# Performance work log

Measured on AMD Instinct MI355X. Metric: run time of the kernel, lower is better.

The kernel has to match this reference:

```python
import jax, jax.numpy as jnp
import numpy as np

B, L, DM, H = 2, 2048, 512, 8
D = DM // H
FACTOR = 5
NUM_K = int(FACTOR * np.ceil(np.log(L)))  # 40
NUM_Q = NUM_K  # q_len == k_len here
EPS = 1e-5


def setup_inputs() -> dict:
    key = jax.random.key(0)
    ks = jax.random.split(key, 12)
    s = DM ** -0.5
    return {
        "q": jax.random.normal(ks[0], (B, L, DM), jnp.float32),
        "k": jax.random.normal(ks[1], (B, L, DM), jnp.float32),
        "v": jax.random.normal(ks[2], (B, L, DM), jnp.float32),
        "Wq": jax.random.normal(ks[3], (DM, DM), jnp.float32) * s,
        "bq": jnp.zeros((DM,), jnp.float32),
        "Wk": jax.random.normal(ks[4], (DM, DM), jnp.float32) * s,
        "bk": jnp.zeros((DM,), jnp.float32),
        "Wv": jax.random.normal(ks[5], (DM, DM), jnp.float32) * s,
        "bv": jnp.zeros((DM,), jnp.float32),
        "gamma": jnp.ones((DM,), jnp.float32),
        "beta": jnp.zeros((DM,), jnp.float32),
        "random_index": jax.random.randint(ks[6], (L, NUM_K), 0, L, jnp.int32),
    }


def _heads(x):
    # [B, L, DM] -> [B, H, L, D]
    return x.reshape(B, L, H, D).transpose(0, 2, 1, 3)


def reference(q, k, v, Wq, bq, Wk, bk, Wv, bv, gamma, beta, random_index):
    qp = _heads(q @ Wq + bq)
    kp = _heads(k @ Wk + bk)
    vp = _heads(v @ Wv + bv)

    # ProbSparse: sample NUM_K keys per query position (shared over batch/head)
    k_samp = kp[:, :, random_index, :]                      # [B,H,L,NUM_K,D]
    pre = jnp.einsum('bhid,bhijd->bhij', qp, k_samp)        # [B,H,L,NUM_K]
    measure = pre.max(-1) - pre.sum(-1) / L                 # sparsity measure [B,H,L]
    _, q_idx = jax.lax.top_k(measure, NUM_Q)                # [B,H,NUM_Q]

    q_sel = jnp.take_along_axis(qp, q_idx[..., None], axis=2)   # [B,H,NUM_Q,D]
    attn = jnp.einsum('bhid,bhjd->bhij', q_sel, kp) * D ** -0.5 # [B,H,NUM_Q,L]
    attn = jax.nn.softmax(attn, axis=-1)                    # dropout = identity (eval)
    out_sel = jnp.einsum('bhij,bhjd->bhid', attn, vp)       # [B,H,NUM_Q,D]

    # use_mask=False path: context is the mean of v over keys
    v_mean = vp.mean(axis=2)                                # [B,H,D]
    context = jnp.broadcast_to(v_mean[:, :, None, :], (B, H, L, D))
    bi = jnp.arange(B)[:, None, None]
    hi = jnp.arange(H)[None, :, None]
    out = context.at[bi, hi, q_idx].set(out_sel)            # scatter selected rows

    out = out.transpose(0, 2, 1, 3).reshape(B, L, DM)
    y = out + q
    mu = y.mean(-1, keepdims=True)
    var = y.var(-1, keepdims=True)
    yn = (y - mu) / jnp.sqrt(var + EPS) * gamma + beta
    return (yn, attn)
```

## Files before the change

### kernel.cpp

```cpp
#include <hip/hip_runtime.h>
#include <math.h>

#define BB 2
#define LL 2048
#define DMM 512
#define HH 8
#define DD 64
#define NUMK 40
#define NUMQ 40
#define LNEPS 1e-5f
#define LSEG 512
#define NLS 4

typedef unsigned short ushort_t;
typedef __attribute__((ext_vector_type(8))) short bf16x8;
typedef __attribute__((ext_vector_type(4))) float f32x4;

__device__ inline ushort_t f2bf(float x) {
    union { float f; unsigned int u; } v; v.f = x;
    unsigned int r = v.u + 0x7fffu + ((v.u >> 16) & 1u);
    return (ushort_t)(r >> 16);
}
__device__ inline float bf2f(ushort_t h) {
    union { unsigned int u; float f; } v; v.u = ((unsigned int)h) << 16;
    return v.f;
}

__global__ __launch_bounds__(256) void convert_x_kernel(
    const float* __restrict__ q, const float* __restrict__ k, const float* __restrict__ v,
    ushort_t* __restrict__ Xh, ushort_t* __restrict__ Xl) {
    const size_t plane = (size_t)BB * LL * DMM;
    const float* X = (blockIdx.y == 0) ? q : (blockIdx.y == 1) ? k : v;
    ushort_t* xh = Xh + plane * blockIdx.y;
    ushort_t* xl = Xl + plane * blockIdx.y;
    const size_t base = ((size_t)blockIdx.x * 256 + threadIdx.x) * 8;
    float4 a = *(const float4*)(X + base);
    float4 b = *(const float4*)(X + base + 4);
    float xs[8] = {a.x, a.y, a.z, a.w, b.x, b.y, b.z, b.w};
    unsigned int hp[4], lp[4];
#pragma unroll
    for (int j = 0; j < 4; ++j) {
        ushort_t h0 = f2bf(xs[2 * j]),     h1 = f2bf(xs[2 * j + 1]);
        ushort_t l0 = f2bf(xs[2 * j] - bf2f(h0));
        ushort_t l1 = f2bf(xs[2 * j + 1] - bf2f(h1));
        hp[j] = (unsigned int)h0 | ((unsigned int)h1 << 16);
        lp[j] = (unsigned int)l0 | ((unsigned int)l1 << 16);
    }
    *(uint4*)(xh + base) = make_uint4(hp[0], hp[1], hp[2], hp[3]);
    *(uint4*)(xl + base) = make_uint4(lp[0], lp[1], lp[2], lp[3]);
}

__global__ __launch_bounds__(256) void convert_w_kernel(
    const float* __restrict__ Wq, const float* __restrict__ Wk, const float* __restrict__ Wv,
    ushort_t* __restrict__ Wht, ushort_t* __restrict__ Wlt) {
    __shared__ float tile[64][65];
    const size_t plane = (size_t)DMM * DMM;
    const float* W = (blockIdx.z == 0) ? Wq : (blockIdx.z == 1) ? Wk : Wv;
    ushort_t* wht = Wht + plane * blockIdx.z;
    ushort_t* wlt = Wlt + plane * blockIdx.z;
    const int n0 = blockIdx.x * 64, k0 = blockIdx.y * 64;
    const int t = threadIdx.x;
    const int d = t & 63, g = t >> 6;
    for (int rr = g; rr < 64; rr += 4)
        tile[rr][d] = W[(size_t)(k0 + rr) * DMM + n0 + d];
    __syncthreads();
    for (int cc = g; cc < 64; cc += 4) {
        float x = tile[d][cc];
        ushort_t hi = f2bf(x);
        ushort_t lo = f2bf(x - bf2f(hi));
        wht[(size_t)(n0 + cc) * DMM + k0 + d] = hi;
        wlt[(size_t)(n0 + cc) * DMM + k0 + d] = lo;
    }
}

__device__ inline void stage_one(const ushort_t* __restrict__ g, ushort_t* lbuf,
                                 int r0, int lane, int k0) {
    const int r = r0 + (lane >> 3);
    const int c = (lane & 7) ^ (r & 7);
    const ushort_t* gp = g + (size_t)r * DMM + k0 + c * 8;
    __builtin_amdgcn_global_load_lds(
        (const __attribute__((address_space(1))) unsigned int*)gp,
        (__attribute__((address_space(3))) unsigned int*)(lbuf + (size_t)r0 * 64),
        16, 0, 0);
}
__device__ inline bf16x8 frag_ld(const ushort_t* buf, int row, int c) {
    const int idx = row * 8 + (c ^ (row & 7));
    return *(const bf16x8*)(buf + idx * 8);
}

__global__ __launch_bounds__(256) void proj_mfma_kernel(
    const ushort_t* __restrict__ Xh, const ushort_t* __restrict__ Xl,
    const ushort_t* __restrict__ Wht, const ushort_t* __restrict__ Wlt,
    const float* __restrict__ bq, const float* __restrict__ bk, const float* __restrict__ bv,
    float* __restrict__ Oq, float* __restrict__ Ok, float* __restrict__ Ov) {
    const int z = blockIdx.z;
    const size_t xplane = (size_t)BB * LL * DMM;
    const size_t wplane = (size_t)DMM * DMM;
    const ushort_t* ah_g = Xh + xplane * z;
    const ushort_t* al_g = Xl + xplane * z;
    const ushort_t* bh_g = Wht + wplane * z;
    const ushort_t* bl_g = Wlt + wplane * z;
    const float* bias = (z == 0) ? bq : (z == 1) ? bk : bv;
    float* Out = (z == 0) ? Oq : (z == 1) ? Ok : Ov;

    __shared__ __align__(16) ushort_t bufAh[64 * 64];
    __shared__ __align__(16) ushort_t bufAl[64 * 64];
    __shared__ __align__(16) ushort_t bufBh[64 * 64];
    __shared__ __align__(16) ushort_t bufBl[64 * 64];

    const int t = threadIdx.x;
    const int lane = t & 63, w = t >> 6;
    const int wm = (w & 1) * 32, wn = (w >> 1) * 32;
    const int m0 = blockIdx.x * 64, j0 = blockIdx.y * 64;

    const ushort_t* A_h = ah_g + (size_t)m0 * DMM;
    const ushort_t* A_l = al_g + (size_t)m0 * DMM;
    const ushort_t* B_h = bh_g + (size_t)j0 * DMM;
    const ushort_t* B_l = bl_g + (size_t)j0 * DMM;

    f32x4 acc[2][2];
#pragma unroll
    for (int i = 0; i < 2; ++i)
#pragma unroll
        for (int j = 0; j < 2; ++j) acc[i][j] = (f32x4){0.f, 0.f, 0.f, 0.f};

    for (int ch = 0; ch < 8; ++ch) {
        const int k0 = ch * 64;
#pragma unroll
        for (int i = 0; i < 2; ++i) {
            const int r0 = (w * 2 + i) * 8;
            stage_one(A_h, bufAh, r0, lane, k0);
            stage_one(A_l, bufAl, r0, lane, k0);
            stage_one(B_h, bufBh, r0, lane, k0);
            stage_one(B_l, bufBl, r0, lane, k0);
        }
        __syncthreads();
#pragma unroll
        for (int ks = 0; ks < 2; ++ks) {
            const int cc = ks * 4 + (lane >> 4);
            bf16x8 fah[2], fal[2], fbh[2], fbl[2];
#pragma unroll
            for (int tm = 0; tm < 2; ++tm) {
                const int row = wm + tm * 16 + (lane & 15);
                fah[tm] = frag_ld(bufAh, row, cc);
                fal[tm] = frag_ld(bufAl, row, cc);
            }
#pragma unroll
            for (int tn = 0; tn < 2; ++tn) {
                const int row = wn + tn * 16 + (lane & 15);
                fbh[tn] = frag_ld(bufBh, row, cc);
                fbl[tn] = frag_ld(bufBl, row, cc);
            }
#pragma unroll
            for (int tm = 0; tm < 2; ++tm)
#pragma unroll
                for (int tn = 0; tn < 2; ++tn) {
                    acc[tm][tn] = __builtin_amdgcn_mfma_f32_16x16x32_bf16(fah[tm], fbh[tn], acc[tm][tn], 0, 0, 0);
                    acc[tm][tn] = __builtin_amdgcn_mfma_f32_16x16x32_bf16(fal[tm], fbh[tn], acc[tm][tn], 0, 0, 0);
                    acc[tm][tn] = __builtin_amdgcn_mfma_f32_16x16x32_bf16(fah[tm], fbl[tn], acc[tm][tn], 0, 0, 0);
                }
        }
        __syncthreads();
    }

#pragma unroll
    for (int tn = 0; tn < 2; ++tn) {
        const int gn = j0 + wn + tn * 16 + (lane & 15);
        const float bvv = bias[gn];
        const int h = gn >> 6, d = gn & 63;
#pragma unroll
        for (int tm = 0; tm < 2; ++tm) {
#pragma unroll
            for (int reg = 0; reg < 4; ++reg) {
                const int gm = m0 + wm + tm * 16 + (lane >> 4) * 4 + reg;
                const int b = gm >> 11, l = gm & (LL - 1);
                Out[(((size_t)(b * HH + h)) * LL + l) * DD + d] = acc[tm][tn][reg] + bvv;
            }
        }
    }
}

__global__ __launch_bounds__(256) void measure_kernel(const float* __restrict__ qp2,
                                                      const float* __restrict__ kp2,
                                                      const int* __restrict__ rnd,
                                                      float* __restrict__ measure) {
    const int t = threadIdx.x;
    const int lane = t & 63;
    const int wv = t >> 6;
    const int g = lane >> 4;
    const int dq = (lane & 15) * 4;
    const int bh = blockIdx.x;
    const int i = blockIdx.y * 16 + wv * 4 + g;
    const float4 qv = *(const float4*)(qp2 + ((size_t)bh * LL + i) * DD + dq);
    const float* kbase = kp2 + (size_t)bh * LL * DD;
    const int* rp = rnd + i * NUMK;
    float mx = -INFINITY, sm = 0.f;
#pragma unroll 8
    for (int j = 0; j < NUMK; ++j) {
        const int row = rp[j];
        const float4 kv = *(const float4*)(kbase + (size_t)row * DD + dq);
        float p = kv.x * qv.x;
        p = fmaf(kv.y, qv.y, p); p = fmaf(kv.z, qv.z, p); p = fmaf(kv.w, qv.w, p);
        p += __shfl_xor(p, 1, 64);
        p += __shfl_xor(p, 2, 64);
        p += __shfl_xor(p, 4, 64);
        p += __shfl_xor(p, 8, 64);
        mx = fmaxf(mx, p);
        sm += p;
    }
    if ((lane & 15) == 0) measure[(size_t)bh * LL + i] = mx - sm * (1.0f / LL);
}

__global__ __launch_bounds__(256) void topk_kernel(const float* __restrict__ measure,
                                                   int* __restrict__ q_idx,
                                                   int* __restrict__ sel_pos) {
    __shared__ unsigned int keys[LL];
    __shared__ int hist[256];
    __shared__ unsigned int prefix_sh;
    __shared__ int need_sh;
    __shared__ unsigned int cval[256];
    __shared__ int cidx[256];
    __shared__ int cnt;
    const int t = threadIdx.x;
    const int bh = blockIdx.x;
    for (int i = t; i < LL; i += 256) {
        const float f = measure[(size_t)bh * LL + i];
        unsigned int u = __float_as_uint(f);
        keys[i] = (u & 0x80000000u) ? ~u : (u | 0x80000000u);
        sel_pos[(size_t)bh * LL + i] = -1;
    }
    if (t == 0) { prefix_sh = 0u; need_sh = NUMQ; cnt = 0; }
    __syncthreads();

    for (int round = 0; round < 4; ++round) {
        const int shift = 24 - round * 8;
        hist[t] = 0;
        __syncthreads();
        const unsigned int pref = prefix_sh;
        const unsigned int mask = (round == 0) ? 0u : (0xFFFFFFFFu << (shift + 8));
        for (int i = t; i < LL; i += 256) {
            const unsigned int key = keys[i];
            if ((key & mask) == pref)
                atomicAdd(&hist[(key >> shift) & 0xFF], 1);
        }
        __syncthreads();
        if (t == 0) {
            const int need = need_sh;
            int acc = 0;
            int v = 255;
            for (; v > 0; --v) {
                if (acc + hist[v] >= need) break;
                acc += hist[v];
            }
            need_sh = need - acc;
            prefix_sh = pref | ((unsigned int)v << shift);
        }
        __syncthreads();
    }
    const unsigned int K40 = prefix_sh;

    for (int i = t; i < LL; i += 256) {
        if (keys[i] >= K40) {
            int p = atomicAdd(&cnt, 1);
            if (p < 256) { cval[p] = keys[i]; cidx[p] = i; }
        }
    }
    __syncthreads();
    int M = cnt; if (M > 256) M = 256;
    for (int i = t; i < M; i += 256) {
        const unsigned int ki = cval[i];
        const int ii = cidx[i];
        int r = 0;
        for (int j = 0; j < M; ++j) {
            const unsigned int kj = cval[j];
            r += (kj > ki || (kj == ki && cidx[j] < ii)) ? 1 : 0;
        }
        if (r < NUMQ) {
            q_idx[bh * NUMQ + r] = ii;
            sel_pos[(size_t)bh * LL + ii] = r;
        }
    }
}

__global__ __launch_bounds__(256) void attn_part_kernel(
    const float* __restrict__ qp2, const float* __restrict__ kp2,
    const float* __restrict__ vp2, const int* __restrict__ q_idx,
    float* __restrict__ attn_out, float* __restrict__ part_m,
    float* __restrict__ part_s, float* __restrict__ part_pv) {
    __shared__ __align__(16) float buf[2][64 * 64];
    __shared__ __align__(16) float sc[4][LSEG];
    __shared__ float pvred[16][68];
    const int t = threadIdx.x;
    const int lane = t & 63, w = t >> 6;
    const int bh = blockIdx.x;
    const int qg = blockIdx.y;
    const int ls = blockIdx.z;
    const int l0 = ls * LSEG;
    const int dseg = lane >> 4;
    const int kk = lane & 15;

    float qrf[4][16];
#pragma unroll
    for (int qq = 0; qq < 4; ++qq) {
        const int qi = q_idx[bh * NUMQ + qg * 4 + qq];
        const float* qrow = qp2 + ((size_t)bh * LL + qi) * DD + dseg * 16;
#pragma unroll
        for (int j = 0; j < 4; ++j) {
            float4 v = *(const float4*)(qrow + j * 4);
            qrf[qq][j * 4 + 0] = v.x * 0.125f;
            qrf[qq][j * 4 + 1] = v.y * 0.125f;
            qrf[qq][j * 4 + 2] = v.z * 0.125f;
            qrf[qq][j * 4 + 3] = v.w * 0.125f;
        }
    }

    const float* kseg = kp2 + ((size_t)bh * LL + l0) * DD;
    const float* vseg = vp2 + ((size_t)bh * LL + l0) * DD;

    auto stage = [&](const float* gsrc, float* lb) {
#pragma unroll
        for (int i = 0; i < 4; ++i) {
            const int instr = w * 4 + i;
            const int r = instr * 4 + (lane >> 4);
            const int cg = (lane & 15) ^ (r & 15);
            const float* gp = gsrc + (size_t)r * DD + cg * 4;
            __builtin_amdgcn_global_load_lds(
                (const __attribute__((address_space(1))) unsigned int*)gp,
                (__attribute__((address_space(3))) unsigned int*)(lb + instr * 256),
                16, 0, 0);
        }
    };

    stage(kseg, buf[0]);
    const int krow = w * 16 + kk;
    for (int c = 0; c < 8; ++c) {
        __syncthreads();
        if (c < 7) stage(kseg + (size_t)(c + 1) * 64 * DD, buf[(c + 1) & 1]);
        const float* lb = buf[c & 1];
        float dot[4] = {0.f, 0.f, 0.f, 0.f};
#pragma unroll
        for (int j = 0; j < 4; ++j) {
            const int cg = dseg * 4 + j;
            const float4 k4 = *(const float4*)(lb + krow * 64 + ((cg ^ (krow & 15)) * 4));
            const float kf[4] = {k4.x, k4.y, k4.z, k4.w};
#pragma unroll
            for (int qq = 0; qq < 4; ++qq)
#pragma unroll
                for (int m = 0; m < 4; ++m)
                    dot[qq] = fmaf(qrf[qq][j * 4 + m], kf[m], dot[qq]);
        }
#pragma unroll
        for (int qq = 0; qq < 4; ++qq) {
            dot[qq] += __shfl_xor(dot[qq], 16, 64);
            dot[qq] += __shfl_xor(dot[qq], 32, 64);
        }
        const float sel = (dseg == 0) ? dot[0] : (dseg == 1) ? dot[1]
                        : (dseg == 2) ? dot[2] : dot[3];
        sc[dseg][c * 64 + krow] = sel;
    }
    stage(vseg, buf[0]);
    __syncthreads();

    const int row = bh * NUMQ + qg * 4 + w;
    {
        float* srow = sc[w];
        float4 v0 = *(float4*)(srow + lane * 8);
        float4 v1 = *(float4*)(srow + lane * 8 + 4);
        float m = fmaxf(fmaxf(fmaxf(v0.x, v0.y), fmaxf(v0.z, v0.w)),
                        fmaxf(fmaxf(v1.x, v1.y), fmaxf(v1.z, v1.w)));
#pragma unroll
        for (int off = 32; off > 0; off >>= 1) m = fmaxf(m, __shfl_xor(m, off, 64));
        v0.x = __expf(v0.x - m); v0.y = __expf(v0.y - m);
        v0.z = __expf(v0.z - m); v0.w = __expf(v0.w - m);
        v1.x = __expf(v1.x - m); v1.y = __expf(v1.y - m);
        v1.z = __expf(v1.z - m); v1.w = __expf(v1.w - m);
        *(float4*)(srow + lane * 8) = v0;
        *(float4*)(srow + lane * 8 + 4) = v1;
        float* arow = attn_out + (size_t)row * LL + l0;
        *(float4*)(arow + lane * 8) = v0;
        *(float4*)(arow + lane * 8 + 4) = v1;
        float s = (v0.x + v0.y + v0.z + v0.w) + (v1.x + v1.y + v1.z + v1.w);
#pragma unroll
        for (int off = 32; off > 0; off >>= 1) s += __shfl_xor(s, off, 64);
        if (lane == 0) {
            part_m[row * NLS + ls] = m;
            part_s[row * NLS + ls] = s;
        }
    }

    const int dq4 = (t & 15) * 4;
    const int grp = t >> 4;
    float4 acc[4];
#pragma unroll
    for (int qq = 0; qq < 4; ++qq) acc[qq] = make_float4(0.f, 0.f, 0.f, 0.f);
    for (int c = 0; c < 8; ++c) {
        __syncthreads();
        if (c < 7) stage(vseg + (size_t)(c + 1) * 64 * DD, buf[(c + 1) & 1]);
        const float* lb = buf[c & 1];
        float pa[4][4];
#pragma unroll
        for (int qq = 0; qq < 4; ++qq)
            *(float4*)&pa[qq][0] = *(const float4*)&sc[qq][c * 64 + grp * 4];
#pragma unroll
        for (int i = 0; i < 4; ++i) {
            const int r = grp * 4 + i;
            const float4 v4 = *(const float4*)(lb + r * 64 + (((t & 15) ^ (r & 15)) * 4));
#pragma unroll
            for (int qq = 0; qq < 4; ++qq) {
                acc[qq].x = fmaf(pa[qq][i], v4.x, acc[qq].x);
                acc[qq].y = fmaf(pa[qq][i], v4.y, acc[qq].y);
                acc[qq].z = fmaf(pa[qq][i], v4.z, acc[qq].z);
                acc[qq].w = fmaf(pa[qq][i], v4.w, acc[qq].w);
            }
        }
    }
#pragma unroll
    for (int qq = 0; qq < 4; ++qq) {
        __syncthreads();
        *(float4*)&pvred[grp][dq4] = acc[qq];
        __syncthreads();
        if (t < DD) {
            float s = 0.f;
#pragma unroll
            for (int u = 0; u < 16; ++u) s += pvred[u][t];
            const int prow = bh * NUMQ + qg * 4 + qq;
            part_pv[((size_t)prow * NLS + ls) * DD + t] = s;
        }
    }
}

__global__ __launch_bounds__(256) void attn_fin_kernel(
    const float* __restrict__ part_m, const float* __restrict__ part_s,
    const float* __restrict__ part_pv, float* __restrict__ attn_out,
    float* __restrict__ out_sel) {
    const int row = blockIdx.x;
    const int t = threadIdx.x;
    float m0 = part_m[row * NLS + 0], m1 = part_m[row * NLS + 1];
    float m2 = part_m[row * NLS + 2], m3 = part_m[row * NLS + 3];
    float M = fmaxf(fmaxf(m0, m1), fmaxf(m2, m3));
    float f[NLS];
    f[0] = __expf(m0 - M); f[1] = __expf(m1 - M);
    f[2] = __expf(m2 - M); f[3] = __expf(m3 - M);
    float T = part_s[row * NLS + 0] * f[0] + part_s[row * NLS + 1] * f[1]
            + part_s[row * NLS + 2] * f[2] + part_s[row * NLS + 3] * f[3];
    const float inv = 1.0f / T;
    float* arow = attn_out + (size_t)row * LL;
    {
        float4 v0 = *(const float4*)&arow[4 * t];
        float4 v1 = *(const float4*)&arow[1024 + 4 * t];
        const float g0 = f[(4 * t) >> 9] * inv;
        const float g1 = f[(1024 + 4 * t) >> 9] * inv;
        v0.x *= g0; v0.y *= g0; v0.z *= g0; v0.w *= g0;
        v1.x *= g1; v1.y *= g1; v1.z *= g1; v1.w *= g1;
        *(float4*)&arow[4 * t] = v0;
        *(float4*)&arow[1024 + 4 * t] = v1;
    }
    if (t < DD) {
        float s = part_pv[((size_t)row * NLS + 0) * DD + t] * f[0]
                + part_pv[((size_t)row * NLS + 1) * DD + t] * f[1]
                + part_pv[((size_t)row * NLS + 2) * DD + t] * f[2]
                + part_pv[((size_t)row * NLS + 3) * DD + t] * f[3];
        out_sel[(size_t)row * DD + t] = s * inv;
    }
}

__global__ __launch_bounds__(256) void vmean1_kernel(const float* __restrict__ vp2,
                                                     float* __restrict__ partial) {
    __shared__ float pv[256];
    const int t = threadIdx.x;
    const int chunk = blockIdx.x & 31;
    const int bh = blockIdx.x >> 5;
    const int d = t & 63, g = t >> 6;
    const int l0 = chunk * 64;
    float acc = 0.f;
    for (int l = l0 + g; l < l0 + 64; l += 4)
        acc += vp2[((size_t)bh * LL + l) * DD + d];
    pv[t] = acc;
    __syncthreads();
    if (t < 64)
        partial[(size_t)blockIdx.x * 64 + t] = pv[t] + pv[64 + t] + pv[128 + t] + pv[192 + t];
}

__global__ __launch_bounds__(64) void vmean2_kernel(const float* __restrict__ partial,
                                                    float* __restrict__ v_mean) {
    const int bh = blockIdx.x;
    const int t = threadIdx.x;
    float s = 0.f;
    for (int c = 0; c < 32; ++c)
        s += partial[((size_t)bh * 32 + c) * 64 + t];
    v_mean[bh * 64 + t] = s * (1.0f / LL);
}

__global__ __launch_bounds__(512) void final_kernel(const float* __restrict__ q_in,
                                                    const int* __restrict__ sel_pos,
                                                    const float* __restrict__ out_sel,
                                                    const float* __restrict__ v_mean,
                                                    const float* __restrict__ gamma,
                                                    const float* __restrict__ beta,
                                                    float* __restrict__ yout) {
    __shared__ float wred[8];
    const int j = threadIdx.x;
    const int lane = j & 63, wv = j >> 6;
    const int tok = blockIdx.x;
    const int b = tok >> 11;
    const int l = tok & (LL - 1);
    const int h = wv, d = lane;
    const int bh = b * HH + h;
    const int p = sel_pos[(size_t)bh * LL + l];
    float val = (p >= 0) ? out_sel[((size_t)bh * NUMQ + p) * DD + d]
                         : v_mean[bh * DD + d];
    float y = val + q_in[(size_t)tok * DMM + j];
    float s = y;
#pragma unroll
    for (int off = 32; off > 0; off >>= 1) s += __shfl_xor(s, off, 64);
    if (lane == 0) wred[wv] = s;
    __syncthreads();
    float tot = 0.f;
#pragma unroll
    for (int u = 0; u < 8; ++u) tot += wred[u];
    float mu = tot * (1.0f / DMM);
    __syncthreads();
    float dv = y - mu;
    float s2 = dv * dv;
#pragma unroll
    for (int off = 32; off > 0; off >>= 1) s2 += __shfl_xor(s2, off, 64);
    if (lane == 0) wred[wv] = s2;
    __syncthreads();
    float tot2 = 0.f;
#pragma unroll
    for (int u = 0; u < 8; ++u) tot2 += wred[u];
    float var = tot2 * (1.0f / DMM);
    float yn = dv * rsqrtf(var + LNEPS) * gamma[j] + beta[j];
    yout[(size_t)tok * DMM + j] = yn;
}

extern "C" void kernel_launch(void* const* d_in, const int* in_sizes, int n_in,
                              void* d_out, int out_size, void* d_ws, size_t ws_size,
                              hipStream_t stream) {
    const float* q     = (const float*)d_in[0];
    const float* k     = (const float*)d_in[1];
    const float* v     = (const float*)d_in[2];
    const float* Wq    = (const float*)d_in[3];
    const float* bq    = (const float*)d_in[4];
    const float* Wk    = (const float*)d_in[5];
    const float* bk    = (const float*)d_in[6];
    const float* Wv    = (const float*)d_in[7];
    const float* bv    = (const float*)d_in[8];
    const float* gamma = (const float*)d_in[9];
    const float* beta  = (const float*)d_in[10];
    const int*   rnd   = (const int*)d_in[11];

    float* ws = (float*)d_ws;
    const size_t proj_sz = (size_t)BB * HH * LL * DD;
    float* qp2     = ws;
    float* kp2     = qp2 + proj_sz;
    float* vp2     = kp2 + proj_sz;
    float* measure = vp2 + proj_sz;
    float* out_sel = measure + (size_t)BB * HH * LL;
    float* v_mean  = out_sel + (size_t)BB * HH * NUMQ * DD;
    float* partial = v_mean + (size_t)BB * HH * DD;
    float* part_m  = partial + (size_t)BB * HH * 32 * 64;
    float* part_s  = part_m + (size_t)BB * HH * NUMQ * NLS;
    float* part_pv = part_s + (size_t)BB * HH * NUMQ * NLS;
    int*   q_idx   = (int*)(part_pv + (size_t)BB * HH * NUMQ * NLS * DD);
    int*   sel_pos = q_idx + BB * HH * NUMQ;
    ushort_t* Xh  = (ushort_t*)(sel_pos + BB * HH * LL);
    ushort_t* Xl  = Xh + 3 * proj_sz;
    ushort_t* Wht = Xl + 3 * proj_sz;
    ushort_t* Wlt = Wht + 3 * (size_t)DMM * DMM;

    float* yn_out   = (float*)d_out;
    float* attn_out = yn_out + (size_t)BB * LL * DMM;

    convert_x_kernel<<<dim3(BB * LL * DMM / (256 * 8), 3), 256, 0, stream>>>(q, k, v, Xh, Xl);
    convert_w_kernel<<<dim3(DMM / 64, DMM / 64, 3), 256, 0, stream>>>(Wq, Wk, Wv, Wht, Wlt);
    proj_mfma_kernel<<<dim3(BB * LL / 64, DMM / 64, 3), 256, 0, stream>>>(
        Xh, Xl, Wht, Wlt, bq, bk, bv, qp2, kp2, vp2);
    vmean1_kernel<<<BB * HH * 32, 256, 0, stream>>>(vp2, partial);
    vmean2_kernel<<<BB * HH, 64, 0, stream>>>(partial, v_mean);
    measure_kernel<<<dim3(BB * HH, LL / 16), 256, 0, stream>>>(qp2, kp2, rnd, measure);
    topk_kernel<<<BB * HH, 256, 0, stream>>>(measure, q_idx, sel_pos);
    attn_part_kernel<<<dim3(BB * HH, NUMQ / 4, NLS), 256, 0, stream>>>(
        qp2, kp2, vp2, q_idx, attn_out, part_m, part_s, part_pv);
    attn_fin_kernel<<<BB * HH * NUMQ, 256, 0, stream>>>(
        part_m, part_s, part_pv, attn_out, out_sel);
    final_kernel<<<BB * LL, 512, 0, stream>>>(q, sel_pos, out_sel, v_mean, gamma, beta, yn_out);
}
```

Before: 218.7 us.

## Enlarge projection GEMM M-tile to 128 and merge v-mean into one kernel

The projection MFMA kernel now computes a 128x64 output tile per block, with each wave handling 64x32, which doubles A-side register tiling and halves how often B tiles are reloaded. This cuts grid size from 1536 to 768 blocks and raises LDS and register use. Separately, the two-stage v-mean reduction becomes a single 1024-thread kernel per batch-head, which removes a launch and the partial buffer but uses only 16 blocks.

```diff
diff --git a/kernel.cpp b/kernel.cpp
--- a/kernel.cpp
+++ b/kernel.cpp
@@ -73,14 +73,14 @@
     }
 }
 
-__device__ inline void stage_one(const ushort_t* __restrict__ g, ushort_t* lbuf,
-                                 int r0, int lane, int k0) {
-    const int r = r0 + (lane >> 3);
+__device__ inline void stage_rows(const ushort_t* __restrict__ g, ushort_t* lbuf,
+                                  int instr, int lane, int k0) {
+    const int r = instr * 8 + (lane >> 3);
     const int c = (lane & 7) ^ (r & 7);
     const ushort_t* gp = g + (size_t)r * DMM + k0 + c * 8;
     __builtin_amdgcn_global_load_lds(
         (const __attribute__((address_space(1))) unsigned int*)gp,
-        (__attribute__((address_space(3))) unsigned int*)(lbuf + (size_t)r0 * 64),
+        (__attribute__((address_space(3))) unsigned int*)(lbuf + (size_t)instr * 512),
         16, 0, 0);
 }
 __device__ inline bf16x8 frag_ld(const ushort_t* buf, int row, int c) {
@@ -103,44 +103,46 @@
     const float* bias = (z == 0) ? bq : (z == 1) ? bk : bv;
     float* Out = (z == 0) ? Oq : (z == 1) ? Ok : Ov;
 
-    __shared__ __align__(16) ushort_t bufAh[64 * 64];
-    __shared__ __align__(16) ushort_t bufAl[64 * 64];
+    __shared__ __align__(16) ushort_t bufAh[128 * 64];
+    __shared__ __align__(16) ushort_t bufAl[128 * 64];
     __shared__ __align__(16) ushort_t bufBh[64 * 64];
     __shared__ __align__(16) ushort_t bufBl[64 * 64];
 
     const int t = threadIdx.x;
     const int lane = t & 63, w = t >> 6;
-    const int wm = (w & 1) * 32, wn = (w >> 1) * 32;
-    const int m0 = blockIdx.x * 64, j0 = blockIdx.y * 64;
+    const int wm = (w & 1) * 64, wn = (w >> 1) * 32;
+    const int m0 = blockIdx.x * 128, j0 = blockIdx.y * 64;
 
     const ushort_t* A_h = ah_g + (size_t)m0 * DMM;
     const ushort_t* A_l = al_g + (size_t)m0 * DMM;
     const ushort_t* B_h = bh_g + (size_t)j0 * DMM;
     const ushort_t* B_l = bl_g + (size_t)j0 * DMM;
 
-    f32x4 acc[2][2];
-#pragma unroll
-    for (int i = 0; i < 2; ++i)
+    f32x4 acc[4][2];
+#pragma unroll
+    for (int i = 0; i < 4; ++i)
 #pragma unroll
         for (int j = 0; j < 2; ++j) acc[i][j] = (f32x4){0.f, 0.f, 0.f, 0.f};
 
     for (int ch = 0; ch < 8; ++ch) {
         const int k0 = ch * 64;
 #pragma unroll
+        for (int i = 0; i < 4; ++i) {
+            stage_rows(A_h, bufAh, w * 4 + i, lane, k0);
+            stage_rows(A_l, bufAl, w * 4 + i, lane, k0);
+        }
+#pragma unroll
         for (int i = 0; i < 2; ++i) {
-            const int r0 = (w * 2 + i) * 8;
-            stage_one(A_h, bufAh, r0, lane, k0);
-            stage_one(A_l, bufAl, r0, lane, k0);
-            stage_one(B_h, bufBh, r0, lane, k0);
-            stage_one(B_l, bufBl, r0, lane, k0);
+            stage_rows(B_h, bufBh, w * 2 + i, lane, k0);
+            stage_rows(B_l, bufBl, w * 2 + i, lane, k0);
         }
         __syncthreads();
 #pragma unroll
         for (int ks = 0; ks < 2; ++ks) {
             const int cc = ks * 4 + (lane >> 4);
-            bf16x8 fah[2], fal[2], fbh[2], fbl[2];
-#pragma unroll
-            for (int tm = 0; tm < 2; ++tm) {
+            bf16x8 fah[4], fal[4], fbh[2], fbl[2];
+#pragma unroll
+            for (int tm = 0; tm < 4; ++tm) {
                 const int row = wm + tm * 16 + (lane & 15);
                 fah[tm] = frag_ld(bufAh, row, cc);
                 fal[tm] = frag_ld(bufAl, row, cc);
@@ -152,7 +154,7 @@
                 fbl[tn] = frag_ld(bufBl, row, cc);
             }
 #pragma unroll
-            for (int tm = 0; tm < 2; ++tm)
+            for (int tm = 0; tm < 4; ++tm)
 #pragma unroll
                 for (int tn = 0; tn < 2; ++tn) {
                     acc[tm][tn] = __builtin_amdgcn_mfma_f32_16x16x32_bf16(fah[tm], fbh[tn], acc[tm][tn], 0, 0, 0);
@@ -169,7 +171,7 @@
         const float bvv = bias[gn];
         const int h = gn >> 6, d = gn & 63;
 #pragma unroll
-        for (int tm = 0; tm < 2; ++tm) {
+        for (int tm = 0; tm < 4; ++tm) {
 #pragma unroll
             for (int reg = 0; reg < 4; ++reg) {
                 const int gm = m0 + wm + tm * 16 + (lane >> 4) * 4 + reg;
@@ -464,31 +466,23 @@
     }
 }
 
-__global__ __launch_bounds__(256) void vmean1_kernel(const float* __restrict__ vp2,
-                                                     float* __restrict__ partial) {
-    __shared__ float pv[256];
-    const int t = threadIdx.x;
-    const int chunk = blockIdx.x & 31;
-    const int bh = blockIdx.x >> 5;
+__global__ __launch_bounds__(1024) void vmean_kernel(const float* __restrict__ vp2,
+                                                     float* __restrict__ v_mean) {
+    __shared__ float pv[1024];
+    const int t = threadIdx.x;
+    const int bh = blockIdx.x;
     const int d = t & 63, g = t >> 6;
-    const int l0 = chunk * 64;
     float acc = 0.f;
-    for (int l = l0 + g; l < l0 + 64; l += 4)
+    for (int l = g; l < LL; l += 16)
         acc += vp2[((size_t)bh * LL + l) * DD + d];
     pv[t] = acc;
     __syncthreads();
-    if (t < 64)
-        partial[(size_t)blockIdx.x * 64 + t] = pv[t] + pv[64 + t] + pv[128 + t] + pv[192 + t];
-}
-
-__global__ __launch_bounds__(64) void vmean2_kernel(const float* __restrict__ partial,
-                                                    float* __restrict__ v_mean) {
-    const int bh = blockIdx.x;
-    const int t = threadIdx.x;
-    float s = 0.f;
-    for (int c = 0; c < 32; ++c)
-        s += partial[((size_t)bh * 32 + c) * 64 + t];
-    v_mean[bh * 64 + t] = s * (1.0f / LL);
+    if (t < 64) {
+        float s = 0.f;
+#pragma unroll
+        for (int u = 0; u < 16; ++u) s += pv[u * 64 + t];
+        v_mean[bh * 64 + t] = s * (1.0f / LL);
+    }
 }
 
 __global__ __launch_bounds__(512) void final_kernel(const float* __restrict__ q_in,
@@ -558,8 +552,7 @@
     float* measure = vp2 + proj_sz;
     float* out_sel = measure + (size_t)BB * HH * LL;
     float* v_mean  = out_sel + (size_t)BB * HH * NUMQ * DD;
-    float* partial = v_mean + (size_t)BB * HH * DD;
-    float* part_m  = partial + (size_t)BB * HH * 32 * 64;
+    float* part_m  = v_mean + (size_t)BB * HH * DD;
     float* part_s  = part_m + (size_t)BB * HH * NUMQ * NLS;
     float* part_pv = part_s + (size_t)BB * HH * NUMQ * NLS;
     int*   q_idx   = (int*)(part_pv + (size_t)BB * HH * NUMQ * NLS * DD);
@@ -574,10 +567,9 @@
 
     convert_x_kernel<<<dim3(BB * LL * DMM / (256 * 8), 3), 256, 0, stream>>>(q, k, v, Xh, Xl);
     convert_w_kernel<<<dim3(DMM / 64, DMM / 64, 3), 256, 0, stream>>>(Wq, Wk, Wv, Wht, Wlt);
-    proj_mfma_kernel<<<dim3(BB * LL / 64, DMM / 64, 3), 256, 0, stream>>>(
+    proj_mfma_kernel<<<dim3(BB * LL / 128, DMM / 64, 3), 256, 0, stream>>>(
         Xh, Xl, Wht, Wlt, bq, bk, bv, qp2, kp2, vp2);
-    vmean1_kernel<<<BB * HH * 32, 256, 0, stream>>>(vp2, partial);
-    vmean2_kernel<<<BB * HH, 64, 0, stream>>>(partial, v_mean);
+    vmean_kernel<<<BB * HH, 1024, 0, stream>>>(vp2, v_mean);
     measure_kernel<<<dim3(BB * HH, LL / 16), 256, 0, stream>>>(qp2, kp2, rnd, measure);
     topk_kernel<<<BB * HH, 256, 0, stream>>>(measure, q_idx, sel_pos);
     attn_part_kernel<<<dim3(BB * HH, NUMQ / 4, NLS), 256, 0, stream>>>(
```

After: 249.8 us. +14.2%, slower.
